# Kernel tuning notes

Hardware: AMD Instinct MI355X
Metric: run time of the kernel (lower is better)

## Reference

```python
import jax, jax.numpy as jnp
import numpy as np

# ---- static configuration (mirrors ConvolutionConfig) ----
B_IMG, C_IN, H, W = 8, 16, 32, 32
C_OUT = 64
KH, KW = 5, 5          # receptive_field
SH, SW = 2, 2          # stride
PH, PW = 2, 2          # padding
N_BITS = 6             # n_inputs_per_node
HIDDEN = [36, 6, 1]    # 6^2, 6^1, 6^0 (tree_depth=2)
INPUT_SIZE = C_IN * KH * KW  # 400
OH = (H + 2 * PH - KH) // SH + 1  # 16
OW = (W + 2 * PW - KW) // SW + 1  # 16


def setup_inputs() -> dict:
    key = jax.random.key(0)
    ks = jax.random.split(key, 7)
    x = jax.random.uniform(ks[0], (B_IMG, C_IN, H, W), dtype=jnp.float32)
    # per-tree random input mappings (6 inputs per LUT node)
    idx0 = jax.random.randint(ks[1], (C_OUT, HIDDEN[0], N_BITS), 0, INPUT_SIZE)
    idx1 = jax.random.randint(ks[2], (C_OUT, HIDDEN[1], N_BITS), 0, HIDDEN[0])
    idx2 = jax.random.randint(ks[3], (C_OUT, HIDDEN[2], N_BITS), 0, HIDDEN[1])
    # raw LUT tables (64 entries), passed through sigmoid in forward
    table0 = jax.random.normal(ks[4], (C_OUT, HIDDEN[0], 64), dtype=jnp.float32)
    table1 = jax.random.normal(ks[5], (C_OUT, HIDDEN[1], 64), dtype=jnp.float32)
    table2 = jax.random.normal(ks[6], (C_OUT, HIDDEN[2], 64), dtype=jnp.float32)
    return {"x": x, "idx0": idx0, "table0": table0, "idx1": idx1,
            "table1": table1, "idx2": idx2, "table2": table2}


def _unfold(x):
    """torch nn.Unfold equivalent -> rows of [B*L, C*KH*KW], c slowest."""
    xp = jnp.pad(x, ((0, 0), (0, 0), (PH, PH), (PW, PW)))
    ri = (jnp.arange(OH) * SH)[:, None] + jnp.arange(KH)[None, :]  # [OH,KH]
    ci = (jnp.arange(OW) * SW)[:, None] + jnp.arange(KW)[None, :]  # [OW,KW]
    # [B, C, OH, OW, KH, KW]
    p = xp[:, :, ri[:, None, :, None], ci[None, :, None, :]]
    p = jnp.transpose(p, (0, 2, 3, 1, 4, 5))  # [B, OH, OW, C, KH, KW]
    return p.reshape(B_IMG * OH * OW, INPUT_SIZE)


def _lut_nodes(g, table):
    """Differentiable LUT node (multilinear interpolation over 2^6 table).
    g: [B, T, N, 6] probabilistic bits in [0,1]; table: [T, N, 64].
    Output: [B, T, N] = sum_a sigmoid(table)[a] * prod_i (g_i if bit_i(a) else 1-g_i).
    Computed by sequential bit contraction to avoid a [B,T,N,64] product tensor.
    """
    T, N = table.shape[0], table.shape[1]
    f = jnp.stack([1.0 - g, g], axis=-1)  # [B,T,N,6,2]
    w = jax.nn.sigmoid(table)             # [T,N,64]
    # contract most-significant bit first
    acc = jnp.einsum('tnkr,btnk->btnr', w.reshape(T, N, 2, 32), f[..., 0, :])
    for b in range(1, N_BITS):
        acc = jnp.einsum('btnkr,btnk->btnr',
                         acc.reshape(acc.shape[0], T, N, 2, -1), f[..., b, :])
    return acc[..., 0]  # [B,T,N]


def reference(x, idx0, table0, idx1, table1, idx2, table2):
    p = _unfold(x)                       # [BP, 400], BP = B*OH*OW
    tind = jnp.arange(C_OUT)[:, None, None]
    # first layer (chunked in torch; mathematically one big gathered layer)
    g0 = p[:, idx0]                      # [BP, C_OUT, 36, 6]
    h0 = _lut_nodes(g0, table0)          # [BP, C_OUT, 36]
    # tree layer 1: 36 -> 6 per tree
    g1 = h0[:, tind, idx1]               # [BP, C_OUT, 6, 6]
    h1 = _lut_nodes(g1, table1)          # [BP, C_OUT, 6]
    # tree layer 2: 6 -> 1 per tree
    g2 = h1[:, tind, idx2]               # [BP, C_OUT, 1, 6]
    h2 = _lut_nodes(g2, table2)[..., 0]  # [BP, C_OUT]
    out = h2.reshape(B_IMG, OH * OW, C_OUT)
    out = jnp.transpose(out, (0, 2, 1)).reshape(B_IMG, C_OUT, OH, OW)
    return out
```

## Files before the change

### kernel.cpp

```cpp
#include <hip/hip_runtime.h>

#define B_IMG 8
#define C_IN  16
#define COUT  64
#define H0    36
#define H1    6
#define NB    6
#define NNODE 43

typedef float f32x2 __attribute__((ext_vector_type(2)));

__device__ __forceinline__ float sigf(float v) { return 1.0f / (1.0f + __expf(-v)); }

__device__ __forceinline__ float lut_contract_reg(const float4 lo4[8], const float4 dd4[8],
                                                  const float g[NB]) {
    f32x2 v[16];
    const float g0 = g[0];
#pragma unroll
    for (int q = 0; q < 8; ++q) {
        v[2*q+0] = (f32x2){lo4[q].x, lo4[q].y} + (f32x2){dd4[q].x, dd4[q].y} * g0;
        v[2*q+1] = (f32x2){lo4[q].z, lo4[q].w} + (f32x2){dd4[q].z, dd4[q].w} * g0;
    }
#pragma unroll
    for (int i = 1; i < 5; ++i) {
        const int vh = 16 >> i;
        const float gi = g[i];
#pragma unroll
        for (int r = 0; r < vh; ++r)
            v[r] += (v[r + vh] - v[r]) * gi;
    }
    return v[0].x + (v[0].y - v[0].x) * g[5];
}

__device__ __forceinline__ void load_tbl_lds(const float* tb, float4 lo4[8], float4 dd4[8]) {
    const float4* t4 = (const float4*)tb;
#pragma unroll
    for (int q = 0; q < 8; ++q) { lo4[q] = t4[q]; dd4[q] = t4[q + 8]; }
}

__global__ __launch_bounds__(512, 4) void lutone_kernel(
    const float* __restrict__ x,
    const int*   __restrict__ idx0,
    const float* __restrict__ t0,
    const int*   __restrict__ idx1,
    const float* __restrict__ t1,
    const int*   __restrict__ idx2,
    const float* __restrict__ t2,
    float*       __restrict__ out)
{
    __shared__ float tblL[NNODE*64];
    __shared__ float h0s[H0*256];
    __shared__ float h1s[H1*256];
    __shared__ int   metaL[H0*NB*2];

    const int tid  = threadIdx.x;
    const int w    = tid >> 6;
    const int lane = tid & 63;
    const int t    = blockIdx.x & 63;
    const int img  = blockIdx.x >> 6;

    for (int e = tid; e < NNODE*32; e += 512) {
        const int node = e >> 5, k = e & 31;
        const float* src = (node < H0)      ? t0 + ((size_t)t*H0 + node)*64
                         : (node < H0+H1)   ? t1 + ((size_t)t*H1 + node - H0)*64
                                            : t2 + (size_t)t*64;
        const float lo = sigf(src[k]);
        const float hi = sigf(src[k + 32]);
        tblL[node*64 + k]      = lo;
        tblL[node*64 + 32 + k] = hi - lo;
    }
    if (tid < H0*NB) {
        const int raw = idx0[(size_t)t*(H0*NB) + tid];
        const int c2  = raw / 25;
        const int rem = raw - 25*c2;
        const int kh  = rem / 5, kw = rem - 5*kh;
        metaL[tid*2 + 0] = c2*1024 + kh*32 + kw - 66;
        metaL[tid*2 + 1] = rem;
    }

    const int* i1base = idx1 + t*(H1*NB);
    unsigned long long umask = 0ull;
#pragma unroll
    for (int j = 0; j < H1*NB; ++j) umask |= 1ull << i1base[j];

    int base[4], vmask[4];
#pragma unroll
    for (int c = 0; c < 4; ++c) {
        const int p  = (c << 6) + lane;
        const int oh = p >> 4, ow = p & 15;
        base[c] = img*16384 + oh*64 + ow*2;
        const int hm = 0x1F ^ ((oh == 0) ? 0x03 : 0) ^ ((oh == 15) ? 0x10 : 0);
        const int wm = 0x1F ^ ((ow == 0) ? 0x03 : 0) ^ ((ow == 15) ? 0x10 : 0);
        int vm = 0;
#pragma unroll
        for (int kh = 0; kh < 5; ++kh)
            vm |= ((hm >> kh) & 1) ? (wm << (5*kh)) : 0;
        vmask[c] = vm;
    }

    int myn0 = -1, myn1 = -1, myn2 = -1, myn3 = -1, myn4 = -1;
    {
        int cnt = 0;
        for (int n = 0; n < H0; ++n) {
            if (!((umask >> n) & 1ull)) continue;
            const int slot = cnt++;
            if ((slot & 7) != w) continue;
            const int k = slot >> 3;
            if      (k == 0) myn0 = n;
            else if (k == 1) myn1 = n;
            else if (k == 2) myn2 = n;
            else if (k == 3) myn3 = n;
            else             myn4 = n;
        }
    }
    __syncthreads();

#define NODE_A(NN)                                                           \
    if ((NN) >= 0) {                                                         \
        const int4* mp = (const int4*)(metaL + (NN)*12);                     \
        const int4 ma = mp[0], mb = mp[1], mc = mp[2];                       \
        float4 lo4[8], dd4[8];                                               \
        load_tbl_lds(tblL + (NN)*64, lo4, dd4);                              \
        _Pragma("unroll")                                                    \
        for (int c = 0; c < 4; ++c) {                                        \
            const int off_[NB] = {ma.x, ma.z, mb.x, mb.z, mc.x, mc.z};       \
            const int rem_[NB] = {ma.y, ma.w, mb.y, mb.w, mc.y, mc.w};       \
            float g[NB];                                                     \
            _Pragma("unroll")                                                \
            for (int i = 0; i < NB; ++i) {                                   \
                const bool ok = ((vmask[c] >> rem_[i]) & 1) != 0;            \
                const float v = x[ok ? (base[c] + off_[i]) : 0];             \
                g[i] = ok ? v : 0.0f;                                        \
            }                                                                \
            h0s[(NN)*256 + (c << 6) + lane] = lut_contract_reg(lo4, dd4, g); \
        }                                                                    \
    }
    NODE_A(myn0)
    NODE_A(myn1)
    NODE_A(myn2)
    NODE_A(myn3)
    NODE_A(myn4)
#undef NODE_A
    __syncthreads();

    if (w < H1) {
        float4 lo4[8], dd4[8];
        load_tbl_lds(tblL + (H0 + w)*64, lo4, dd4);
        const int* i1 = idx1 + ((size_t)t*H1 + w)*NB;
        const int s0 = i1[0], s1 = i1[1], s2 = i1[2];
        const int s3 = i1[3], s4 = i1[4], s5 = i1[5];
#pragma unroll
        for (int c = 0; c < 3; ++c) {
            const int px = (c << 6) + lane;
            float g[NB];
            g[0] = h0s[s0*256 + px]; g[1] = h0s[s1*256 + px]; g[2] = h0s[s2*256 + px];
            g[3] = h0s[s3*256 + px]; g[4] = h0s[s4*256 + px]; g[5] = h0s[s5*256 + px];
            h1s[w*256 + px] = lut_contract_reg(lo4, dd4, g);
        }
    } else {
        const int nb0 = (w == 6) ? 0 : 3;
        const int px  = (3 << 6) + lane;
#pragma unroll
        for (int k = 0; k < 3; ++k) {
            const int n = nb0 + k;
            float4 lo4[8], dd4[8];
            load_tbl_lds(tblL + (H0 + n)*64, lo4, dd4);
            const int* i1 = idx1 + ((size_t)t*H1 + n)*NB;
            float g[NB];
            g[0] = h0s[i1[0]*256 + px]; g[1] = h0s[i1[1]*256 + px];
            g[2] = h0s[i1[2]*256 + px]; g[3] = h0s[i1[3]*256 + px];
            g[4] = h0s[i1[4]*256 + px]; g[5] = h0s[i1[5]*256 + px];
            h1s[n*256 + px] = lut_contract_reg(lo4, dd4, g);
        }
    }
    __syncthreads();

    if (w < 4) {
        float4 lo4[8], dd4[8];
        load_tbl_lds(tblL + (H0 + H1)*64, lo4, dd4);
        const int* i2 = idx2 + (size_t)t*NB;
        const int px = (w << 6) + lane;
        float g[NB];
#pragma unroll
        for (int i = 0; i < NB; ++i) g[i] = h1s[i2[i]*256 + px];
        out[((size_t)img*COUT + t)*256 + px] = lut_contract_reg(lo4, dd4, g);
    }
}

extern "C" void kernel_launch(void* const* d_in, const int* in_sizes, int n_in,
                              void* d_out, int out_size, void* d_ws, size_t ws_size,
                              hipStream_t stream) {
    const float* x      = (const float*)d_in[0];
    const int*   idx0   = (const int*)  d_in[1];
    const float* table0 = (const float*)d_in[2];
    const int*   idx1   = (const int*)  d_in[3];
    const float* table1 = (const float*)d_in[4];
    const int*   idx2   = (const int*)  d_in[5];
    const float* table2 = (const float*)d_in[6];
    float* out = (float*)d_out;

    lutone_kernel<<<COUT * B_IMG, 512, 0, stream>>>(
        x, idx0, table0, idx1, table1, idx2, table2, out);
}
```

Before: 21.68 us.

## Split each image-tree block into two pixel halves with 256-thread blocks

Splits the 256 output pixels of each (image, tree) pair across two blocks of 256 threads instead of one block of 512, which doubles the grid and halves the LDS scratch per block. The first layer now gathers two pixel chunks per node, and the input loads are interleaved with the table loads so memory latency overlaps with work. Table sigmoid preprocessing now uses float4 loads, and the idx1/idx2 indices are staged in LDS. The cost is that every block repeats the table sigmoid and metadata setup, so that per-tree setup work is duplicated across the two halves.

```diff
diff --git a/kernel.cpp b/kernel.cpp
--- a/kernel.cpp
+++ b/kernel.cpp
@@ -11,6 +11,9 @@
 typedef float f32x2 __attribute__((ext_vector_type(2)));
 
 __device__ __forceinline__ float sigf(float v) { return 1.0f / (1.0f + __expf(-v)); }
+__device__ __forceinline__ float4 sig4(float4 a) {
+    return make_float4(sigf(a.x), sigf(a.y), sigf(a.z), sigf(a.w));
+}
 
 __device__ __forceinline__ float lut_contract_reg(const float4 lo4[8], const float4 dd4[8],
                                                   const float g[NB]) {
@@ -38,7 +41,7 @@
     for (int q = 0; q < 8; ++q) { lo4[q] = t4[q]; dd4[q] = t4[q + 8]; }
 }
 
-__global__ __launch_bounds__(512, 4) void lutone_kernel(
+__global__ __launch_bounds__(256) void lutone_kernel(
     const float* __restrict__ x,
     const int*   __restrict__ idx0,
     const float* __restrict__ t0,
@@ -49,25 +52,34 @@
     float*       __restrict__ out)
 {
     __shared__ float tblL[NNODE*64];
-    __shared__ float h0s[H0*256];
-    __shared__ float h1s[H1*256];
+    __shared__ float h0s[H0*128];
+    __shared__ float h1s[H1*128];
     __shared__ int   metaL[H0*NB*2];
+    __shared__ int   idx1L[H1*NB];
+    __shared__ int   idx2L[NB];
 
     const int tid  = threadIdx.x;
     const int w    = tid >> 6;
     const int lane = tid & 63;
-    const int t    = blockIdx.x & 63;
-    const int img  = blockIdx.x >> 6;
-
-    for (int e = tid; e < NNODE*32; e += 512) {
-        const int node = e >> 5, k = e & 31;
-        const float* src = (node < H0)      ? t0 + ((size_t)t*H0 + node)*64
-                         : (node < H0+H1)   ? t1 + ((size_t)t*H1 + node - H0)*64
-                                            : t2 + (size_t)t*64;
-        const float lo = sigf(src[k]);
-        const float hi = sigf(src[k + 32]);
-        tblL[node*64 + k]      = lo;
-        tblL[node*64 + 32 + k] = hi - lo;
+    const int b    = blockIdx.x;
+    const int t    = b & 63;
+    const int img  = (b >> 6) & 7;
+    const int half = b >> 9;
+
+    {
+        float4* tbl4 = (float4*)tblL;
+        for (int e = tid; e < NNODE*8; e += 256) {
+            const int node = e >> 3, q = e & 7;
+            const float* src = (node < H0)      ? t0 + ((size_t)t*H0 + node)*64
+                             : (node < H0+H1)   ? t1 + ((size_t)t*H1 + node - H0)*64
+                                                : t2 + (size_t)t*64;
+            const float4* s4 = (const float4*)src;
+            const float4 lo = sig4(s4[q]);
+            const float4 hi = sig4(s4[q + 8]);
+            tbl4[node*16 + q]     = lo;
+            tbl4[node*16 + 8 + q] = make_float4(hi.x - lo.x, hi.y - lo.y,
+                                                hi.z - lo.z, hi.w - lo.w);
+        }
     }
     if (tid < H0*NB) {
         const int raw = idx0[(size_t)t*(H0*NB) + tid];
@@ -77,16 +89,18 @@
         metaL[tid*2 + 0] = c2*1024 + kh*32 + kw - 66;
         metaL[tid*2 + 1] = rem;
     }
+    if (tid < H1*NB) idx1L[tid] = idx1[(size_t)t*(H1*NB) + tid];
+    if (tid < NB)    idx2L[tid] = idx2[(size_t)t*NB + tid];
 
     const int* i1base = idx1 + t*(H1*NB);
     unsigned long long umask = 0ull;
 #pragma unroll
     for (int j = 0; j < H1*NB; ++j) umask |= 1ull << i1base[j];
 
-    int base[4], vmask[4];
-#pragma unroll
-    for (int c = 0; c < 4; ++c) {
-        const int p  = (c << 6) + lane;
+    int base[2], vmask[2];
+#pragma unroll
+    for (int c = 0; c < 2; ++c) {
+        const int p  = half*128 + (c << 6) + lane;
         const int oh = p >> 4, ow = p & 15;
         base[c] = img*16384 + oh*64 + ow*2;
         const int hm = 0x1F ^ ((oh == 0) ? 0x03 : 0) ^ ((oh == 15) ? 0x10 : 0);
@@ -98,92 +112,85 @@
         vmask[c] = vm;
     }
 
-    int myn0 = -1, myn1 = -1, myn2 = -1, myn3 = -1, myn4 = -1;
+    int myn0=-1, myn1=-1, myn2=-1, myn3=-1, myn4=-1, myn5=-1, myn6=-1, myn7=-1, myn8=-1;
     {
         int cnt = 0;
         for (int n = 0; n < H0; ++n) {
             if (!((umask >> n) & 1ull)) continue;
             const int slot = cnt++;
-            if ((slot & 7) != w) continue;
-            const int k = slot >> 3;
-            if      (k == 0) myn0 = n;
-            else if (k == 1) myn1 = n;
-            else if (k == 2) myn2 = n;
-            else if (k == 3) myn3 = n;
-            else             myn4 = n;
+            if ((slot & 3) != w) continue;
+            switch (slot >> 2) {
+                case 0: myn0 = n; break;
+                case 1: myn1 = n; break;
+                case 2: myn2 = n; break;
+                case 3: myn3 = n; break;
+                case 4: myn4 = n; break;
+                case 5: myn5 = n; break;
+                case 6: myn6 = n; break;
+                case 7: myn7 = n; break;
+                default: myn8 = n; break;
+            }
         }
     }
     __syncthreads();
 
+#define GATH(dst, C)                                                         \
+    _Pragma("unroll")                                                        \
+    for (int i = 0; i < NB; ++i) {                                           \
+        const bool ok = ((vmask[C] >> rem_[i]) & 1) != 0;                    \
+        const float v = x[ok ? (base[C] + off_[i]) : 0];                     \
+        dst[i] = ok ? v : 0.0f;                                              \
+    }
 #define NODE_A(NN)                                                           \
     if ((NN) >= 0) {                                                         \
         const int4* mp = (const int4*)(metaL + (NN)*12);                     \
         const int4 ma = mp[0], mb = mp[1], mc = mp[2];                       \
+        const int off_[NB] = {ma.x, ma.z, mb.x, mb.z, mc.x, mc.z};           \
+        const int rem_[NB] = {ma.y, ma.w, mb.y, mb.w, mc.y, mc.w};           \
+        float gA[NB], gB[NB];                                                \
+        GATH(gA, 0)                                                          \
         float4 lo4[8], dd4[8];                                               \
         load_tbl_lds(tblL + (NN)*64, lo4, dd4);                              \
-        _Pragma("unroll")                                                    \
-        for (int c = 0; c < 4; ++c) {                                        \
-            const int off_[NB] = {ma.x, ma.z, mb.x, mb.z, mc.x, mc.z};       \
-            const int rem_[NB] = {ma.y, ma.w, mb.y, mb.w, mc.y, mc.w};       \
-            float g[NB];                                                     \
-            _Pragma("unroll")                                                \
-            for (int i = 0; i < NB; ++i) {                                   \
-                const bool ok = ((vmask[c] >> rem_[i]) & 1) != 0;            \
-                const float v = x[ok ? (base[c] + off_[i]) : 0];             \
-                g[i] = ok ? v : 0.0f;                                        \
-            }                                                                \
-            h0s[(NN)*256 + (c << 6) + lane] = lut_contract_reg(lo4, dd4, g); \
-        }                                                                    \
+        GATH(gB, 1)                                                          \
+        h0s[(NN)*128 + lane]      = lut_contract_reg(lo4, dd4, gA);          \
+        h0s[(NN)*128 + 64 + lane] = lut_contract_reg(lo4, dd4, gB);          \
     }
     NODE_A(myn0)
     NODE_A(myn1)
     NODE_A(myn2)
     NODE_A(myn3)
     NODE_A(myn4)
+    NODE_A(myn5)
+    NODE_A(myn6)
+    NODE_A(myn7)
+    NODE_A(myn8)
 #undef NODE_A
+#undef GATH
     __syncthreads();
 
-    if (w < H1) {
+#pragma unroll
+    for (int j = 0; j < 3; ++j) {
+        const int u = 3*w + j;
+        const int n = u >> 1, c = u & 1;
         float4 lo4[8], dd4[8];
-        load_tbl_lds(tblL + (H0 + w)*64, lo4, dd4);
-        const int* i1 = idx1 + ((size_t)t*H1 + w)*NB;
-        const int s0 = i1[0], s1 = i1[1], s2 = i1[2];
-        const int s3 = i1[3], s4 = i1[4], s5 = i1[5];
-#pragma unroll
-        for (int c = 0; c < 3; ++c) {
-            const int px = (c << 6) + lane;
-            float g[NB];
-            g[0] = h0s[s0*256 + px]; g[1] = h0s[s1*256 + px]; g[2] = h0s[s2*256 + px];
-            g[3] = h0s[s3*256 + px]; g[4] = h0s[s4*256 + px]; g[5] = h0s[s5*256 + px];
-            h1s[w*256 + px] = lut_contract_reg(lo4, dd4, g);
-        }
-    } else {
-        const int nb0 = (w == 6) ? 0 : 3;
-        const int px  = (3 << 6) + lane;
-#pragma unroll
-        for (int k = 0; k < 3; ++k) {
-            const int n = nb0 + k;
-            float4 lo4[8], dd4[8];
-            load_tbl_lds(tblL + (H0 + n)*64, lo4, dd4);
-            const int* i1 = idx1 + ((size_t)t*H1 + n)*NB;
-            float g[NB];
-            g[0] = h0s[i1[0]*256 + px]; g[1] = h0s[i1[1]*256 + px];
-            g[2] = h0s[i1[2]*256 + px]; g[3] = h0s[i1[3]*256 + px];
-            g[4] = h0s[i1[4]*256 + px]; g[5] = h0s[i1[5]*256 + px];
-            h1s[n*256 + px] = lut_contract_reg(lo4, dd4, g);
-        }
+        load_tbl_lds(tblL + (H0 + n)*64, lo4, dd4);
+        const int* i1 = idx1L + n*NB;
+        const int px = (c << 6) + lane;
+        float g[NB];
+#pragma unroll
+        for (int i = 0; i < NB; ++i) g[i] = h0s[i1[i]*128 + px];
+        h1s[n*128 + px] = lut_contract_reg(lo4, dd4, g);
     }
     __syncthreads();
 
-    if (w < 4) {
+    if (w < 2) {
         float4 lo4[8], dd4[8];
         load_tbl_lds(tblL + (H0 + H1)*64, lo4, dd4);
-        const int* i2 = idx2 + (size_t)t*NB;
         const int px = (w << 6) + lane;
         float g[NB];
 #pragma unroll
-        for (int i = 0; i < NB; ++i) g[i] = h1s[i2[i]*256 + px];
-        out[((size_t)img*COUT + t)*256 + px] = lut_contract_reg(lo4, dd4, g);
+        for (int i = 0; i < NB; ++i) g[i] = h1s[idx2L[i]*128 + px];
+        out[((size_t)img*COUT + t)*256 + half*128 + px] = lut_contract_reg(lo4, dd4, g);
     }
 }
 
@@ -199,6 +206,6 @@
     const float* table2 = (const float*)d_in[6];
     float* out = (float*)d_out;
 
-    lutone_kernel<<<COUT * B_IMG, 512, 0, stream>>>(
+    lutone_kernel<<<COUT * B_IMG * 2, 256, 0, stream>>>(
         x, idx0, table0, idx1, table1, idx2, table2, out);
 }
```

Result: slower. 23.90 us (+10.2%).

## Load and sigmoid LUT tables directly into registers instead of staging in LDS

Applied to the files above, without the earlier changes.

Removes the block-wide LDS staging pass for all 43 sigmoided tables. Each wave now reads its node's raw table from global memory as float4 and applies sigmoid in registers. Layer-1 work moves from a split layout (6 waves doing 3 chunks, 2 waves covering the last chunk) to 6 waves each doing all 4 chunks. The idx1/idx2 indices are cached in LDS. The launch-bounds occupancy hint is also dropped. In exchange, sigmoid work is repeated per wave (per block, 4x for the final table), global loads sit on each wave's critical path, and layer 1 uses fewer waves.

```diff
diff --git a/kernel.cpp b/kernel.cpp
--- a/kernel.cpp
+++ b/kernel.cpp
@@ -6,7 +6,6 @@
 #define H0    36
 #define H1    6
 #define NB    6
-#define NNODE 43
 
 typedef float f32x2 __attribute__((ext_vector_type(2)));
 
@@ -32,13 +31,21 @@
     return v[0].x + (v[0].y - v[0].x) * g[5];
 }
 
-__device__ __forceinline__ void load_tbl_lds(const float* tb, float4 lo4[8], float4 dd4[8]) {
-    const float4* t4 = (const float4*)tb;
+__device__ __forceinline__ void load_sig_tbl(const float* __restrict__ tb,
+                                             float4 lo4[8], float4 dd4[8]) {
+    const float4* tp = (const float4*)tb;
 #pragma unroll
-    for (int q = 0; q < 8; ++q) { lo4[q] = t4[q]; dd4[q] = t4[q + 8]; }
+    for (int q = 0; q < 8; ++q) {
+        const float4 a = tp[q], b = tp[q + 8];
+        float4 l, d;
+        l.x = sigf(a.x); l.y = sigf(a.y); l.z = sigf(a.z); l.w = sigf(a.w);
+        d.x = sigf(b.x) - l.x; d.y = sigf(b.y) - l.y;
+        d.z = sigf(b.z) - l.z; d.w = sigf(b.w) - l.w;
+        lo4[q] = l; dd4[q] = d;
+    }
 }
 
-__global__ __launch_bounds__(512, 4) void lutone_kernel(
+__global__ __launch_bounds__(512) void lutone_kernel(
     const float* __restrict__ x,
     const int*   __restrict__ idx0,
     const float* __restrict__ t0,
@@ -48,10 +55,11 @@
     const float* __restrict__ t2,
     float*       __restrict__ out)
 {
-    __shared__ float tblL[NNODE*64];
     __shared__ float h0s[H0*256];
     __shared__ float h1s[H1*256];
     __shared__ int   metaL[H0*NB*2];
+    __shared__ int   idx1L[H1*NB];
+    __shared__ int   idx2L[NB];
 
     const int tid  = threadIdx.x;
     const int w    = tid >> 6;
@@ -59,16 +67,6 @@
     const int t    = blockIdx.x & 63;
     const int img  = blockIdx.x >> 6;
 
-    for (int e = tid; e < NNODE*32; e += 512) {
-        const int node = e >> 5, k = e & 31;
-        const float* src = (node < H0)      ? t0 + ((size_t)t*H0 + node)*64
-                         : (node < H0+H1)   ? t1 + ((size_t)t*H1 + node - H0)*64
-                                            : t2 + (size_t)t*64;
-        const float lo = sigf(src[k]);
-        const float hi = sigf(src[k + 32]);
-        tblL[node*64 + k]      = lo;
-        tblL[node*64 + 32 + k] = hi - lo;
-    }
     if (tid < H0*NB) {
         const int raw = idx0[(size_t)t*(H0*NB) + tid];
         const int c2  = raw / 25;
@@ -77,6 +75,8 @@
         metaL[tid*2 + 0] = c2*1024 + kh*32 + kw - 66;
         metaL[tid*2 + 1] = rem;
     }
+    if (tid < H1*NB) idx1L[tid] = idx1[(size_t)t*(H1*NB) + tid];
+    if (tid < NB)    idx2L[tid] = idx2[(size_t)t*NB + tid];
 
     const int* i1base = idx1 + t*(H1*NB);
     unsigned long long umask = 0ull;
@@ -119,12 +119,12 @@
     if ((NN) >= 0) {                                                         \
         const int4* mp = (const int4*)(metaL + (NN)*12);                     \
         const int4 ma = mp[0], mb = mp[1], mc = mp[2];                       \
+        const int off_[NB] = {ma.x, ma.z, mb.x, mb.z, mc.x, mc.z};           \
+        const int rem_[NB] = {ma.y, ma.w, mb.y, mb.w, mc.y, mc.w};           \
         float4 lo4[8], dd4[8];                                               \
-        load_tbl_lds(tblL + (NN)*64, lo4, dd4);                              \
+        load_sig_tbl(t0 + ((size_t)t*H0 + (NN))*64, lo4, dd4);               \
         _Pragma("unroll")                                                    \
         for (int c = 0; c < 4; ++c) {                                        \
-            const int off_[NB] = {ma.x, ma.z, mb.x, mb.z, mc.x, mc.z};       \
-            const int rem_[NB] = {ma.y, ma.w, mb.y, mb.w, mc.y, mc.w};       \
             float g[NB];                                                     \
             _Pragma("unroll")                                                \
             for (int i = 0; i < NB; ++i) {                                   \
@@ -145,44 +145,28 @@
 
     if (w < H1) {
         float4 lo4[8], dd4[8];
-        load_tbl_lds(tblL + (H0 + w)*64, lo4, dd4);
-        const int* i1 = idx1 + ((size_t)t*H1 + w)*NB;
+        load_sig_tbl(t1 + ((size_t)t*H1 + w)*64, lo4, dd4);
+        const int* i1 = idx1L + w*NB;
         const int s0 = i1[0], s1 = i1[1], s2 = i1[2];
         const int s3 = i1[3], s4 = i1[4], s5 = i1[5];
 #pragma unroll
-        for (int c = 0; c < 3; ++c) {
+        for (int c = 0; c < 4; ++c) {
             const int px = (c << 6) + lane;
             float g[NB];
             g[0] = h0s[s0*256 + px]; g[1] = h0s[s1*256 + px]; g[2] = h0s[s2*256 + px];
             g[3] = h0s[s3*256 + px]; g[4] = h0s[s4*256 + px]; g[5] = h0s[s5*256 + px];
             h1s[w*256 + px] = lut_contract_reg(lo4, dd4, g);
         }
-    } else {
-        const int nb0 = (w == 6) ? 0 : 3;
-        const int px  = (3 << 6) + lane;
-#pragma unroll
-        for (int k = 0; k < 3; ++k) {
-            const int n = nb0 + k;
-            float4 lo4[8], dd4[8];
-            load_tbl_lds(tblL + (H0 + n)*64, lo4, dd4);
-            const int* i1 = idx1 + ((size_t)t*H1 + n)*NB;
-            float g[NB];
-            g[0] = h0s[i1[0]*256 + px]; g[1] = h0s[i1[1]*256 + px];
-            g[2] = h0s[i1[2]*256 + px]; g[3] = h0s[i1[3]*256 + px];
-            g[4] = h0s[i1[4]*256 + px]; g[5] = h0s[i1[5]*256 + px];
-            h1s[n*256 + px] = lut_contract_reg(lo4, dd4, g);
-        }
     }
     __syncthreads();
 
     if (w < 4) {
         float4 lo4[8], dd4[8];
-        load_tbl_lds(tblL + (H0 + H1)*64, lo4, dd4);
-        const int* i2 = idx2 + (size_t)t*NB;
+        load_sig_tbl(t2 + (size_t)t*64, lo4, dd4);
         const int px = (w << 6) + lane;
         float g[NB];
 #pragma unroll
-        for (int i = 0; i < NB; ++i) g[i] = h1s[i2[i]*256 + px];
+        for (int i = 0; i < NB; ++i) g[i] = h1s[idx2L[i]*256 + px];
         out[((size_t)img*COUT + t)*256 + px] = lut_contract_reg(lo4, dd4, g);
     }
 }
```

New measurement: 53.65 us. +147.5%, slower.
